# Kernel optimization log

Measured on AMD Instinct MI355X. Metric: run time of the kernel, lower is better.

Reference implementation:

```python
import jax, jax.numpy as jnp
import numpy as np

NF = 64  # n_features
NL = 3   # n_layers


def setup_inputs() -> dict:
    key = jax.random.key(0)
    ks = jax.random.split(key, 16)
    B, G, P = 4, 512, 512
    obs = jax.random.randint(ks[0], (B, G, P), 0, 3).astype(jnp.float32)

    def w(k, shape, fan_in):
        return (jax.random.normal(k, shape, jnp.float32) / np.sqrt(fan_in)).astype(jnp.float32)

    return {
        "obs": obs,
        "W_init_g": w(ks[1], (1, NF), 1),          # node_init_embedding_layer_g Linear(1,64)
        "W_init_p": w(ks[2], (1, NF), 1),
        "W_ee_g": w(ks[3], (1, NF - 1), 1),        # edge_embedding_NN (n_obs_in_p -> 63)
        "W_ef_g": w(ks[4], (NF, NF), NF),          # edge_feature_NN (64 -> 64)
        "W_ee_p": w(ks[5], (1, NF - 1), 1),
        "W_ef_p": w(ks[6], (NF, NF), NF),
        "W_msg_g": w(ks[7], (NL, 2 * NF, NF), 2 * NF),
        "W_upd_g": w(ks[8], (NL, 2 * NF, NF), 2 * NF),
        "W_msg_p": w(ks[9], (NL, 2 * NF, NF), 2 * NF),
        "W_upd_p": w(ks[10], (NL, 2 * NF, NF), 2 * NF),
        "W_pool_g": w(ks[11], (NF, NF), NF),
        "W_pool_p": w(ks[12], (NF, NF), NF),
        "W_ro": w(ks[13], (2 * NF, 1), 2 * NF),    # readout Linear(128,1,bias=True)
        "b_ro": jnp.zeros((1,), jnp.float32),
    }


def _norms(a):
    # torch get_normalisation is under no_grad
    n = jax.lax.stop_gradient(jnp.sum(a != 0, axis=-1, keepdims=True).astype(a.dtype))
    return n, jnp.where(n == 0, 1.0, n)


def _edge_emb(node_feat_opp, adj, norm, nf1, W_ee, W_ef):
    # node_feat_opp: [B,C,1], adj: [B,R,C] -> edge tensor [B,R,C,1]
    mask = (adj != 0).astype(adj.dtype)
    ef = node_feat_opp[:, None, :, :] * mask[..., None]          # [B,R,C,1]
    ee = jax.nn.relu(jnp.einsum('brci,ie->brce', ef, W_ee))      # [B,R,C,63]
    emb = ee.sum(axis=2) / nf1                                   # [B,R,63]
    x = jnp.concatenate([emb, norm / jnp.max(nf1)], axis=-1)     # [B,R,64]
    return jax.nn.relu(x @ W_ef)


def reference(obs, W_init_g, W_init_p, W_ee_g, W_ef_g, W_ee_p, W_ef_p,
              W_msg_g, W_upd_g, W_msg_p, W_upd_p, W_pool_g, W_pool_p, W_ro, b_ro):
    relu = jax.nn.relu
    adj = obs                                  # n_obs_in_g == 1 -> no leading node features
    adjT = jnp.swapaxes(adj, -1, -2)
    B, G, P = adj.shape
    norm_g, nf1_g = _norms(adj)
    norm_p, nf1_p = _norms(adjT)
    nf_g = norm_g / P                          # node_features_g [B,G,1]
    nf_p = norm_p / G                          # node_features_p [B,P,1]
    h_g = relu(nf_g @ W_init_g)                # [B,G,64]
    h_p = relu(nf_p @ W_init_p)                # [B,P,64]
    e_g = _edge_emb(nf_p, adj, norm_g, nf1_g, W_ee_g, W_ef_g)
    e_p = _edge_emb(nf_g, adjT, norm_p, nf1_p, W_ee_p, W_ef_p)
    for i in range(NL):
        agg_g = (adj @ h_p) / nf1_g
        agg_p = (adjT @ h_g) / nf1_p
        m_g = relu(jnp.concatenate([agg_g, e_g], axis=-1) @ W_msg_g[i])
        m_p = relu(jnp.concatenate([agg_p, e_p], axis=-1) @ W_msg_p[i])
        h_g_new = relu(jnp.concatenate([h_g, m_g], axis=-1) @ W_upd_g[i])
        h_p_new = relu(jnp.concatenate([h_p, m_p], axis=-1) @ W_upd_p[i])
        h_g, h_p = h_g_new, h_p_new
    hp_g = (h_g.sum(axis=1) / G) @ W_pool_g    # [B,64]
    hp_p = (h_p.sum(axis=1) / P) @ W_pool_p
    hp = relu(hp_g + hp_p)
    f_pooled = jnp.broadcast_to(hp[:, None, :], h_g.shape)
    feats = relu(jnp.concatenate([f_pooled, h_g], axis=-1))      # [B,G,128]
    out = feats @ W_ro + b_ro                  # [B,G,1]
    return out[..., 0]                         # torch .squeeze() -> [B,G]
```

## Files before the change

kernel.cpp:

```cpp
#include <hip/hip_runtime.h>

#define NF 64

#define OFF_U       8194
#define OFF_NPG     9216
#define OFF_NPP     25600
#define OFF_HA_G    41984
#define OFF_HA_P    173056
#define OFF_HB_G    304128
#define OFF_HB_P    435200
#define OFF_EG      566272
#define OFF_EP      697344
#define OFF_AFRAG   2162688
#define OFF_HFA     3211264
#define OFF_HFB     3735552
#define OFF_WF      4259840
#define OFF_HPART   4358144

typedef __attribute__((ext_vector_type(8))) short bf16x8;
typedef __attribute__((ext_vector_type(4))) float f32x4;

static __device__ __forceinline__ float wave_sum(float v) {
    for (int off = 32; off; off >>= 1) v += __shfl_down(v, off, 64);
    return v;
}
static __device__ __forceinline__ float wave_max(float v) {
    for (int off = 32; off; off >>= 1) v = fmaxf(v, __shfl_down(v, off, 64));
    return v;
}
static __device__ __forceinline__ unsigned short f2bf(float x) {
    unsigned u = __float_as_uint(x);
    return (unsigned short)((u + 0x7FFFu + ((u >> 16) & 1u)) >> 16);
}

__global__ __launch_bounds__(256) void k_prep(const float* __restrict__ obs,
        float* __restrict__ ws,
        const float* __restrict__ Wm_g, const float* __restrict__ Wu_g,
        const float* __restrict__ Wm_p, const float* __restrict__ Wu_p,
        const float* __restrict__ Wee_g, const float* __restrict__ Wef_g,
        const float* __restrict__ Wee_p, const float* __restrict__ Wef_p) {
    __shared__ float tile[64][65];
    __shared__ float cc[4][64];
    int b = blockIdx.y, t = threadIdx.x;
    int tg = blockIdx.x >> 3, tp = blockIdx.x & 7;
    int g0 = tg * 64, p0 = tp * 64;
    int c = t & 63, q = t >> 6;
    const float* src = obs + ((size_t)b * 512 + g0) * 512 + p0;
    float colcnt = 0.f;
#pragma unroll
    for (int i = 0; i < 16; ++i) {
        int r = q + 4 * i;
        float v = src[(size_t)r * 512 + c];
        tile[r][c] = v;
        bool nz = (v != 0.f);
        colcnt += nz ? 1.f : 0.f;
        unsigned long long mask = __ballot(nz);
        if (c == 0)
            ws[OFF_NPG + tp * 2048 + b * 512 + g0 + r] = (float)__popcll(mask);
    }
    cc[q][c] = colcnt;
    __syncthreads();
    if (q == 0)
        ws[OFF_NPP + tg * 2048 + b * 512 + p0 + c] =
            cc[0][c] + cc[1][c] + cc[2][c] + cc[3][c];
    int ri = c & 15, kq = c >> 4;
    unsigned short* afg = (unsigned short*)(ws + OFF_AFRAG);
    unsigned short* afp = afg + 1048576;
    int rt_g = b * 32 + tg * 4 + q;
    int rt_p = b * 32 + tp * 4 + q;
#pragma unroll
    for (int ks2 = 0; ks2 < 2; ++ks2) {
        int ks_g = tp * 2 + ks2;
        int ks_p = tg * 2 + ks2;
        bf16x8 og, op;
#pragma unroll
        for (int i = 0; i < 8; ++i) {
            og[i] = (short)f2bf(tile[q * 16 + ri][ks2 * 32 + kq * 8 + i]);
            op[i] = (short)f2bf(tile[ks2 * 32 + kq * 8 + i][q * 16 + ri]);
        }
        *(bf16x8*)(afg + ((size_t)(rt_g * 16 + ks_g) * 64 + c) * 8) = og;
        *(bf16x8*)(afp + ((size_t)(rt_p * 16 + ks_p) * 64 + c) * 8) = op;
    }
    int lin = b * 64 + blockIdx.x;
    if (lin < 48) {
        int mat = lin >> 2, ks2 = lin & 3;
        int side = mat / 6, m = (mat / 3) & 1, layer = mat % 3;
        const float* W = (side ? (m ? Wu_p : Wm_p) : (m ? Wu_g : Wm_g)) + layer * 8192;
        int ftq = t >> 6, lane = t & 63;
        int f = ftq * 16 + (lane & 15);
        int kbase = ks2 * 32 + ((lane >> 4) & 3) * 8;
        bf16x8 oh, ol;
#pragma unroll
        for (int i = 0; i < 8; ++i) {
            float v = W[(kbase + i) * 64 + f];
            unsigned short hi = f2bf(v);
            oh[i] = (short)hi;
            ol[i] = (short)f2bf(v - __uint_as_float((unsigned)hi << 16));
        }
        unsigned short* WF = (unsigned short*)(ws + OFF_WF);
        *(bf16x8*)(WF + (((size_t)(mat * 2 + 0) * 4 + ks2) * 4 + ftq) * 512 + lane * 8) = oh;
        *(bf16x8*)(WF + (((size_t)(mat * 2 + 1) * 4 + ks2) * 4 + ftq) * 512 + lane * 8) = ol;
    } else if (lin == 48 && t < 128) {
        int side = t >> 6, f = t & 63;
        const float* Wee = side ? Wee_p : Wee_g;
        const float* Wef = side ? Wef_p : Wef_g;
        float u = 0.f;
#pragma unroll
        for (int e = 0; e < 63; ++e) u += fmaxf(Wee[e], 0.f) * Wef[e * 64 + f];
        ws[OFF_U + t] = u;
    }
}

__global__ __launch_bounds__(256) void k_init(float* __restrict__ ws,
        const float* __restrict__ Wi_g, const float* __restrict__ Wi_p,
        const float* __restrict__ Wef_g, const float* __restrict__ Wef_p) {
    __shared__ float normall[2048];
    __shared__ float nopp[512];
    __shared__ float redm[4];
    __shared__ float sred[4][16];
    __shared__ float s_l[16];
    int bid = blockIdx.x, side = bid >> 7, rt = bid & 127;
    int lr0 = rt * 16, b = rt >> 5;
    int t = threadIdx.x, lane = t & 63, w = t >> 6;
    const float* pown = ws + (side ? OFF_NPP : OFF_NPG);
    const float* popp = ws + (side ? OFF_NPG : OFF_NPP) + b * 512;
#pragma unroll
    for (int i = 0; i < 8; ++i) {
        int r = t + 256 * i;
        float s = 0.f;
#pragma unroll
        for (int j = 0; j < 8; ++j) s += pown[j * 2048 + r];
        normall[r] = s;
    }
#pragma unroll
    for (int i = 0; i < 2; ++i) {
        int r = t + 256 * i;
        float s = 0.f;
#pragma unroll
        for (int j = 0; j < 8; ++j) s += popp[j * 2048 + r];
        nopp[r] = s;
    }
    __syncthreads();
    float m = 0.f;
#pragma unroll
    for (int i = 0; i < 8; ++i) m = fmaxf(m, normall[t + 256 * i]);
    m = wave_max(m);
    if (lane == 0) redm[w] = m;
    const unsigned short* af = (const unsigned short*)(ws + OFF_AFRAG)
                               + (size_t)side * 1048576;
    int kq = lane >> 4;
    float sacc = 0.f;
#pragma unroll
    for (int kk = 0; kk < 4; ++kk) {
        int ks = w * 4 + kk;
        bf16x8 a = *(const bf16x8*)(af + ((size_t)(rt * 16 + ks) * 64 + lane) * 8);
#pragma unroll
        for (int i = 0; i < 8; ++i)
            if (a[i] != 0) sacc += nopp[ks * 32 + kq * 8 + i];
    }
    sacc += __shfl_xor(sacc, 16, 64);
    sacc += __shfl_xor(sacc, 32, 64);
    if (lane < 16) sred[w][lane] = sacc;
    __syncthreads();
    float mxs = fmaxf(fmaxf(redm[0], redm[1]), fmaxf(redm[2], redm[3]));
    if (t < 16)
        s_l[t] = (sred[0][t] + sred[1][t] + sred[2][t] + sred[3][t]) * (1.f / 512.f);
    __syncthreads();
    float maxnf = fmaxf(mxs, 1.f);
    const float* Wi = side ? Wi_p : Wi_g;
    const float* Wef = side ? Wef_p : Wef_g;
    int ff = lane;
    float Uv = ws[OFF_U + side * 64 + ff];
    float wef63 = Wef[63 * 64 + ff];
    float wiv = Wi[ff];
    unsigned short hi4[4], lo4[4];
#pragma unroll
    for (int q = 0; q < 4; ++q) {
        int r = w * 4 + q, lr = lr0 + r;
        float norm = normall[lr];
        float nf1 = norm > 0.f ? norm : 1.f;
        float h = fmaxf(norm * (1.f / 512.f) * wiv, 0.f);
        ws[(side ? OFF_HA_P : OFF_HA_G) + (size_t)lr * 64 + ff] = h;
        unsigned short hh = f2bf(h);
        hi4[q] = hh;
        lo4[q] = f2bf(h - __uint_as_float((unsigned)hh << 16));
        float A = s_l[r] / nf1;
        float C = norm / maxnf;
        float e = fmaxf(A * Uv + C * wef63, 0.f);
        ws[(side ? OFF_EP : OFF_EG) + (size_t)lr * 64 + ff] = e;
    }
    int k0 = (rt & 31) * 16 + w * 4;
    int ks_h = k0 >> 5;
    int lane2 = (ff & 15) | (((k0 >> 3) & 3) << 4);
    int ft = ff >> 4;
    size_t fidx = (((size_t)(b * 4 + ft) * 16 + ks_h) * 64 + lane2) * 8 + (k0 & 7);
    unsigned short* hf = (unsigned short*)(ws + OFF_HFA) + (size_t)side * 2 * 262144;
    uint2 vh, vl;
    vh.x = (unsigned)hi4[0] | ((unsigned)hi4[1] << 16);
    vh.y = (unsigned)hi4[2] | ((unsigned)hi4[3] << 16);
    vl.x = (unsigned)lo4[0] | ((unsigned)lo4[1] << 16);
    vl.y = (unsigned)lo4[2] | ((unsigned)lo4[3] << 16);
    *(uint2*)(hf + fidx) = vh;
    *(uint2*)(hf + 262144 + fidx) = vl;
}

__global__ __launch_bounds__(256) void k_layer(float* __restrict__ ws, int layer,
        int hin_g, int hin_p, int hout_g, int hout_p, int fin, int fout, int do_pool) {
    __shared__ float xe[16][68], xh[16][68], xa[16][68], xm[16][68];
    __shared__ float nrm16[16];
    __shared__ float psum[4][64];
    int bid = blockIdx.x, side = bid >> 7, rt = bid & 127;
    int lr0 = rt * 16, b = rt >> 5;
    int t = threadIdx.x, lane = t & 63;
    int ft = __builtin_amdgcn_readfirstlane(t >> 6);

    {
        int r = t >> 4, c4 = (t & 15) * 4;
        *(float4*)&xe[r][c4] = *(const float4*)(ws + (side ? OFF_EP : OFF_EG)
                                                + (size_t)(lr0 + r) * 64 + c4);
        *(float4*)&xh[r][c4] = *(const float4*)(ws + (side ? hin_p : hin_g)
                                                + (size_t)(lr0 + r) * 64 + c4);
        if (t < 16) {
            const float* po = ws + (side ? OFF_NPP : OFF_NPG) + lr0 + t;
            float s = 0.f;
#pragma unroll
            for (int j = 0; j < 8; ++j) s += po[j * 2048];
            nrm16[t] = fmaxf(s, 1.f);
        }
    }
    __syncthreads();

    const unsigned short* af = (const unsigned short*)(ws + OFF_AFRAG)
                               + (size_t)side * 1048576;
    const unsigned short* hfh = (const unsigned short*)(ws + fin)
                                + (size_t)(1 - side) * 2 * 262144;
    const unsigned short* hfl = hfh + 262144;
    f32x4 acc = {0.f, 0.f, 0.f, 0.f};
#pragma unroll
    for (int ks = 0; ks < 16; ++ks) {
        bf16x8 a = *(const bf16x8*)(af + ((size_t)(rt * 16 + ks) * 64 + lane) * 8);
        size_t bi = ((((size_t)b * 4 + ft) * 16 + ks) * 64 + lane) * 8;
        bf16x8 bh = *(const bf16x8*)(hfh + bi);
        bf16x8 bl = *(const bf16x8*)(hfl + bi);
        acc = __builtin_amdgcn_mfma_f32_16x16x32_bf16(a, bh, acc, 0, 0, 0);
        acc = __builtin_amdgcn_mfma_f32_16x16x32_bf16(a, bl, acc, 0, 0, 0);
    }
    {
        int c = lane & 15, rq = (lane >> 4) * 4, f = ft * 16 + c;
#pragma unroll
        for (int j = 0; j < 4; ++j)
            xa[rq + j][f] = acc[j] / nrm16[rq + j];
    }
    __syncthreads();

    const unsigned short* WF = (const unsigned short*)(ws + OFF_WF);
    int mat_msg = (side * 2 + 0) * 3 + layer;
    int mat_upd = (side * 2 + 1) * 3 + layer;
    int ar = lane & 15, koff = ((lane >> 4) & 3) * 8;

    f32x4 mc = {0.f, 0.f, 0.f, 0.f};
#pragma unroll
    for (int ks2 = 0; ks2 < 4; ++ks2) {
        const float* src = (ks2 < 2) ? &xa[ar][ks2 * 32 + koff]
                                     : &xe[ar][(ks2 - 2) * 32 + koff];
        float4 lo4 = *(const float4*)src;
        float4 hi4 = *(const float4*)(src + 4);
        bf16x8 xhf, xlf;
        {
            float xv[8] = {lo4.x, lo4.y, lo4.z, lo4.w, hi4.x, hi4.y, hi4.z, hi4.w};
#pragma unroll
            for (int i = 0; i < 8; ++i) {
                unsigned short hh = f2bf(xv[i]);
                xhf[i] = (short)hh;
                xlf[i] = (short)f2bf(xv[i] - __uint_as_float((unsigned)hh << 16));
            }
        }
        bf16x8 wh = *(const bf16x8*)(WF + (((size_t)(mat_msg * 2 + 0) * 4 + ks2) * 4 + ft) * 512 + lane * 8);
        bf16x8 wl = *(const bf16x8*)(WF + (((size_t)(mat_msg * 2 + 1) * 4 + ks2) * 4 + ft) * 512 + lane * 8);
        mc = __builtin_amdgcn_mfma_f32_16x16x32_bf16(xhf, wh, mc, 0, 0, 0);
        mc = __builtin_amdgcn_mfma_f32_16x16x32_bf16(xlf, wh, mc, 0, 0, 0);
        mc = __builtin_amdgcn_mfma_f32_16x16x32_bf16(xhf, wl, mc, 0, 0, 0);
    }
    {
        int c = lane & 15, rq = (lane >> 4) * 4, f = ft * 16 + c;
#pragma unroll
        for (int j = 0; j < 4; ++j) xm[rq + j][f] = fmaxf(mc[j], 0.f);
    }
    __syncthreads();

    f32x4 uc = {0.f, 0.f, 0.f, 0.f};
#pragma unroll
    for (int ks2 = 0; ks2 < 4; ++ks2) {
        const float* src = (ks2 < 2) ? &xh[ar][ks2 * 32 + koff]
                                     : &xm[ar][(ks2 - 2) * 32 + koff];
        float4 lo4 = *(const float4*)src;
        float4 hi4 = *(const float4*)(src + 4);
        bf16x8 xhf, xlf;
        {
            float xv[8] = {lo4.x, lo4.y, lo4.z, lo4.w, hi4.x, hi4.y, hi4.z, hi4.w};
#pragma unroll
            for (int i = 0; i < 8; ++i) {
                unsigned short hh = f2bf(xv[i]);
                xhf[i] = (short)hh;
                xlf[i] = (short)f2bf(xv[i] - __uint_as_float((unsigned)hh << 16));
            }
        }
        bf16x8 wh = *(const bf16x8*)(WF + (((size_t)(mat_upd * 2 + 0) * 4 + ks2) * 4 + ft) * 512 + lane * 8);
        bf16x8 wl = *(const bf16x8*)(WF + (((size_t)(mat_upd * 2 + 1) * 4 + ks2) * 4 + ft) * 512 + lane * 8);
        uc = __builtin_amdgcn_mfma_f32_16x16x32_bf16(xhf, wh, uc, 0, 0, 0);
        uc = __builtin_amdgcn_mfma_f32_16x16x32_bf16(xlf, wh, uc, 0, 0, 0);
        uc = __builtin_amdgcn_mfma_f32_16x16x32_bf16(xhf, wl, uc, 0, 0, 0);
    }
    {
        int c = lane & 15, rq = (lane >> 4) * 4, f = ft * 16 + c;
        int hout = side ? hout_p : hout_g;
        float s4 = 0.f;
        unsigned short hi4[4], lo4[4];
#pragma unroll
        for (int j = 0; j < 4; ++j) {
            float hv = fmaxf(uc[j], 0.f);
            ws[hout + (size_t)(lr0 + rq + j) * 64 + f] = hv;
            unsigned short hh = f2bf(hv);
            hi4[j] = hh;
            lo4[j] = f2bf(hv - __uint_as_float((unsigned)hh << 16));
            s4 += hv;
        }
        int k0 = (rt & 31) * 16 + rq;
        int ks_h = k0 >> 5;
        int lane2 = (f & 15) | (((k0 >> 3) & 3) << 4);
        size_t fidx = (((size_t)(b * 4 + ft) * 16 + ks_h) * 64 + lane2) * 8 + (k0 & 7);
        unsigned short* hf = (unsigned short*)(ws + fout) + (size_t)side * 2 * 262144;
        uint2 vh, vl;
        vh.x = (unsigned)hi4[0] | ((unsigned)hi4[1] << 16);
        vh.y = (unsigned)hi4[2] | ((unsigned)hi4[3] << 16);
        vl.x = (unsigned)lo4[0] | ((unsigned)lo4[1] << 16);
        vl.y = (unsigned)lo4[2] | ((unsigned)lo4[3] << 16);
        *(uint2*)(hf + fidx) = vh;
        *(uint2*)(hf + 262144 + fidx) = vl;
        if (do_pool) {
            psum[lane >> 4][f] = s4;
            __syncthreads();
            if (t < 64)
                ws[OFF_HPART + bid * 64 + t] =
                    psum[0][t] + psum[1][t] + psum[2][t] + psum[3][t];
        }
    }
}

__global__ __launch_bounds__(256) void k_out(const float* __restrict__ Wpg,
                                             const float* __restrict__ Wpp,
                                             const float* __restrict__ Wro,
                                             const float* __restrict__ bro,
                                             const float* __restrict__ ws,
                                             float* __restrict__ out) {
    __shared__ float hp[128];
    __shared__ float c1s;
    int bid = blockIdx.x;
    int row0 = bid * 256, b = row0 >> 9;
    int t = threadIdx.x;
    if (t < 128) {
        int sd = t >> 6, k = t & 63;
        const float* q = ws + OFF_HPART + (size_t)(sd * 128 + b * 32) * 64 + k;
        float s = 0.f;
#pragma unroll
        for (int i = 0; i < 32; ++i) s += q[i * 64];
        hp[t] = s;
    }
    __syncthreads();
    if (t < 64) {
        float vg = 0.f, vp = 0.f;
#pragma unroll 4
        for (int k = 0; k < 64; ++k) {
            vg += (hp[k] * (1.f / 512.f)) * Wpg[k * 64 + t];
            vp += (hp[64 + k] * (1.f / 512.f)) * Wpp[k * 64 + t];
        }
        float hv = fmaxf(vg + vp, 0.f);
        float c = wave_sum(hv * Wro[t]);
        if (t == 0) c1s = c + bro[0];
    }
    __syncthreads();
    int idx = row0 + t;
    const float4* hrow = (const float4*)(ws + OFF_HB_G + (size_t)idx * 64);
    float s = 0.f;
#pragma unroll
    for (int k4 = 0; k4 < 16; ++k4) {
        float4 h4 = hrow[k4];
        s += h4.x * Wro[64 + k4 * 4 + 0];
        s += h4.y * Wro[64 + k4 * 4 + 1];
        s += h4.z * Wro[64 + k4 * 4 + 2];
        s += h4.w * Wro[64 + k4 * 4 + 3];
    }
    out[idx] = c1s + s;
}

extern "C" void kernel_launch(void* const* d_in, const int* in_sizes, int n_in,
                              void* d_out, int out_size, void* d_ws, size_t ws_size,
                              hipStream_t stream) {
    const float* obs   = (const float*)d_in[0];
    const float* Wi_g  = (const float*)d_in[1];
    const float* Wi_p  = (const float*)d_in[2];
    const float* Wee_g = (const float*)d_in[3];
    const float* Wef_g = (const float*)d_in[4];
    const float* Wee_p = (const float*)d_in[5];
    const float* Wef_p = (const float*)d_in[6];
    const float* Wm_g  = (const float*)d_in[7];
    const float* Wu_g  = (const float*)d_in[8];
    const float* Wm_p  = (const float*)d_in[9];
    const float* Wu_p  = (const float*)d_in[10];
    const float* Wpg   = (const float*)d_in[11];
    const float* Wpp   = (const float*)d_in[12];
    const float* Wro   = (const float*)d_in[13];
    const float* bro   = (const float*)d_in[14];
    float* ws  = (float*)d_ws;
    float* out = (float*)d_out;

    k_prep<<<dim3(64, 4), 256, 0, stream>>>(obs, ws, Wm_g, Wu_g, Wm_p, Wu_p,
                                            Wee_g, Wef_g, Wee_p, Wef_p);
    k_init<<<256, 256, 0, stream>>>(ws, Wi_g, Wi_p, Wef_g, Wef_p);

    k_layer<<<256, 256, 0, stream>>>(ws, 0, OFF_HA_G, OFF_HA_P, OFF_HB_G, OFF_HB_P,
                                     OFF_HFA, OFF_HFB, 0);
    k_layer<<<256, 256, 0, stream>>>(ws, 1, OFF_HB_G, OFF_HB_P, OFF_HA_G, OFF_HA_P,
                                     OFF_HFB, OFF_HFA, 0);
    k_layer<<<256, 256, 0, stream>>>(ws, 2, OFF_HA_G, OFF_HA_P, OFF_HB_G, OFF_HB_P,
                                     OFF_HFA, OFF_HFB, 1);

    k_out<<<8, 256, 0, stream>>>(Wpg, Wpp, Wro, bro, ws, out);
}
```

Baseline: 54.31 us.

## Fuse layer 0 into init using rank-one structure of initial embeddings

Because the initial node embeddings are relu(norm/N * W_init), the layer-0 aggregation adj @ h_opp reduces to a weighted sum of opposite-side norms times relu(W_init_opp). That scalar is accumulated alongside the existing edge-embedding reduction, and the layer-0 message and update MFMA matmuls run inside the init kernel. This removes one full layer kernel and its adjacency matmul and launch. It assumes the opposite initial embedding is rank-one, which holds because the norms are non-negative.

Measured after the change: 46.88 us, median of 2. -13.7%, faster.

```diff
diff --git a/kernel.cpp b/kernel.cpp
--- a/kernel.cpp
+++ b/kernel.cpp
@@ -111,14 +111,15 @@
     }
 }
 
-__global__ __launch_bounds__(256) void k_init(float* __restrict__ ws,
+__global__ __launch_bounds__(256) void k_init_l0(float* __restrict__ ws,
         const float* __restrict__ Wi_g, const float* __restrict__ Wi_p,
         const float* __restrict__ Wef_g, const float* __restrict__ Wef_p) {
     __shared__ float normall[2048];
     __shared__ float nopp[512];
     __shared__ float redm[4];
-    __shared__ float sred[4][16];
-    __shared__ float s_l[16];
+    __shared__ float sred[4][16], wred[4][16];
+    __shared__ float s_l[16], w_l[16];
+    __shared__ float xe[16][68], xh[16][68], xa[16][68], xm[16][68];
     int bid = blockIdx.x, side = bid >> 7, rt = bid & 127;
     int lr0 = rt * 16, b = rt >> 5;
     int t = threadIdx.x, lane = t & 63, w = t >> 6;
@@ -149,59 +150,141 @@
     const unsigned short* af = (const unsigned short*)(ws + OFF_AFRAG)
                                + (size_t)side * 1048576;
     int kq = lane >> 4;
-    float sacc = 0.f;
+    float sacc = 0.f, wacc = 0.f;
 #pragma unroll
     for (int kk = 0; kk < 4; ++kk) {
         int ks = w * 4 + kk;
         bf16x8 a = *(const bf16x8*)(af + ((size_t)(rt * 16 + ks) * 64 + lane) * 8);
 #pragma unroll
         for (int i = 0; i < 8; ++i)
-            if (a[i] != 0) sacc += nopp[ks * 32 + kq * 8 + i];
+            if (a[i] != 0) {
+                float nv = nopp[ks * 32 + kq * 8 + i];
+                sacc += nv;
+                float av = __uint_as_float((unsigned)(unsigned short)a[i] << 16);
+                wacc += av * nv;
+            }
     }
     sacc += __shfl_xor(sacc, 16, 64);
     sacc += __shfl_xor(sacc, 32, 64);
-    if (lane < 16) sred[w][lane] = sacc;
+    wacc += __shfl_xor(wacc, 16, 64);
+    wacc += __shfl_xor(wacc, 32, 64);
+    if (lane < 16) { sred[w][lane] = sacc; wred[w][lane] = wacc; }
     __syncthreads();
     float mxs = fmaxf(fmaxf(redm[0], redm[1]), fmaxf(redm[2], redm[3]));
-    if (t < 16)
+    if (t < 16) {
         s_l[t] = (sred[0][t] + sred[1][t] + sred[2][t] + sred[3][t]) * (1.f / 512.f);
+        w_l[t] = (wred[0][t] + wred[1][t] + wred[2][t] + wred[3][t]) * (1.f / 512.f);
+    }
     __syncthreads();
     float maxnf = fmaxf(mxs, 1.f);
-    const float* Wi = side ? Wi_p : Wi_g;
+    const float* Wi_own = side ? Wi_p : Wi_g;
+    const float* Wi_opp = side ? Wi_g : Wi_p;
     const float* Wef = side ? Wef_p : Wef_g;
     int ff = lane;
     float Uv = ws[OFF_U + side * 64 + ff];
     float wef63 = Wef[63 * 64 + ff];
-    float wiv = Wi[ff];
-    unsigned short hi4[4], lo4[4];
+    float wiv = Wi_own[ff];
+    float wio = fmaxf(Wi_opp[ff], 0.f);
 #pragma unroll
     for (int q = 0; q < 4; ++q) {
         int r = w * 4 + q, lr = lr0 + r;
         float norm = normall[lr];
         float nf1 = norm > 0.f ? norm : 1.f;
         float h = fmaxf(norm * (1.f / 512.f) * wiv, 0.f);
-        ws[(side ? OFF_HA_P : OFF_HA_G) + (size_t)lr * 64 + ff] = h;
-        unsigned short hh = f2bf(h);
-        hi4[q] = hh;
-        lo4[q] = f2bf(h - __uint_as_float((unsigned)hh << 16));
+        xh[r][ff] = h;
         float A = s_l[r] / nf1;
         float C = norm / maxnf;
         float e = fmaxf(A * Uv + C * wef63, 0.f);
         ws[(side ? OFF_EP : OFF_EG) + (size_t)lr * 64 + ff] = e;
-    }
-    int k0 = (rt & 31) * 16 + w * 4;
-    int ks_h = k0 >> 5;
-    int lane2 = (ff & 15) | (((k0 >> 3) & 3) << 4);
-    int ft = ff >> 4;
-    size_t fidx = (((size_t)(b * 4 + ft) * 16 + ks_h) * 64 + lane2) * 8 + (k0 & 7);
-    unsigned short* hf = (unsigned short*)(ws + OFF_HFA) + (size_t)side * 2 * 262144;
-    uint2 vh, vl;
-    vh.x = (unsigned)hi4[0] | ((unsigned)hi4[1] << 16);
-    vh.y = (unsigned)hi4[2] | ((unsigned)hi4[3] << 16);
-    vl.x = (unsigned)lo4[0] | ((unsigned)lo4[1] << 16);
-    vl.y = (unsigned)lo4[2] | ((unsigned)lo4[3] << 16);
-    *(uint2*)(hf + fidx) = vh;
-    *(uint2*)(hf + 262144 + fidx) = vl;
+        xe[r][ff] = e;
+        xa[r][ff] = w_l[r] * wio / nf1;
+    }
+    __syncthreads();
+
+    int ft = __builtin_amdgcn_readfirstlane(w);
+    const unsigned short* WF = (const unsigned short*)(ws + OFF_WF);
+    int mat_msg = (side * 2 + 0) * 3 + 0;
+    int mat_upd = (side * 2 + 1) * 3 + 0;
+    int ar = lane & 15, koff = ((lane >> 4) & 3) * 8;
+
+    f32x4 mc = {0.f, 0.f, 0.f, 0.f};
+#pragma unroll
+    for (int ks2 = 0; ks2 < 4; ++ks2) {
+        const float* src = (ks2 < 2) ? &xa[ar][ks2 * 32 + koff]
+                                     : &xe[ar][(ks2 - 2) * 32 + koff];
+        float4 lo4 = *(const float4*)src;
+        float4 hi4 = *(const float4*)(src + 4);
+        bf16x8 xhf, xlf;
+        {
+            float xv[8] = {lo4.x, lo4.y, lo4.z, lo4.w, hi4.x, hi4.y, hi4.z, hi4.w};
+#pragma unroll
+            for (int i = 0; i < 8; ++i) {
+                unsigned short hh = f2bf(xv[i]);
+                xhf[i] = (short)hh;
+                xlf[i] = (short)f2bf(xv[i] - __uint_as_float((unsigned)hh << 16));
+            }
+        }
+        bf16x8 wh = *(const bf16x8*)(WF + (((size_t)(mat_msg * 2 + 0) * 4 + ks2) * 4 + ft) * 512 + lane * 8);
+        bf16x8 wl = *(const bf16x8*)(WF + (((size_t)(mat_msg * 2 + 1) * 4 + ks2) * 4 + ft) * 512 + lane * 8);
+        mc = __builtin_amdgcn_mfma_f32_16x16x32_bf16(xhf, wh, mc, 0, 0, 0);
+        mc = __builtin_amdgcn_mfma_f32_16x16x32_bf16(xlf, wh, mc, 0, 0, 0);
+        mc = __builtin_amdgcn_mfma_f32_16x16x32_bf16(xhf, wl, mc, 0, 0, 0);
+    }
+    {
+        int c = lane & 15, rq = (lane >> 4) * 4, f = ft * 16 + c;
+#pragma unroll
+        for (int j = 0; j < 4; ++j) xm[rq + j][f] = fmaxf(mc[j], 0.f);
+    }
+    __syncthreads();
+
+    f32x4 uc = {0.f, 0.f, 0.f, 0.f};
+#pragma unroll
+    for (int ks2 = 0; ks2 < 4; ++ks2) {
+        const float* src = (ks2 < 2) ? &xh[ar][ks2 * 32 + koff]
+                                     : &xm[ar][(ks2 - 2) * 32 + koff];
+        float4 lo4 = *(const float4*)src;
+        float4 hi4 = *(const float4*)(src + 4);
+        bf16x8 xhf, xlf;
+        {
+            float xv[8] = {lo4.x, lo4.y, lo4.z, lo4.w, hi4.x, hi4.y, hi4.z, hi4.w};
+#pragma unroll
+            for (int i = 0; i < 8; ++i) {
+                unsigned short hh = f2bf(xv[i]);
+                xhf[i] = (short)hh;
+                xlf[i] = (short)f2bf(xv[i] - __uint_as_float((unsigned)hh << 16));
+            }
+        }
+        bf16x8 wh = *(const bf16x8*)(WF + (((size_t)(mat_upd * 2 + 0) * 4 + ks2) * 4 + ft) * 512 + lane * 8);
+        bf16x8 wl = *(const bf16x8*)(WF + (((size_t)(mat_upd * 2 + 1) * 4 + ks2) * 4 + ft) * 512 + lane * 8);
+        uc = __builtin_amdgcn_mfma_f32_16x16x32_bf16(xhf, wh, uc, 0, 0, 0);
+        uc = __builtin_amdgcn_mfma_f32_16x16x32_bf16(xlf, wh, uc, 0, 0, 0);
+        uc = __builtin_amdgcn_mfma_f32_16x16x32_bf16(xhf, wl, uc, 0, 0, 0);
+    }
+    {
+        int c = lane & 15, rq = (lane >> 4) * 4, f = ft * 16 + c;
+        int hout = side ? OFF_HB_P : OFF_HB_G;
+        unsigned short hi4[4], lo4b[4];
+#pragma unroll
+        for (int j = 0; j < 4; ++j) {
+            float hv = fmaxf(uc[j], 0.f);
+            ws[hout + (size_t)(lr0 + rq + j) * 64 + f] = hv;
+            unsigned short hh = f2bf(hv);
+            hi4[j] = hh;
+            lo4b[j] = f2bf(hv - __uint_as_float((unsigned)hh << 16));
+        }
+        int k0 = (rt & 31) * 16 + rq;
+        int ks_h = k0 >> 5;
+        int lane2 = (f & 15) | (((k0 >> 3) & 3) << 4);
+        size_t fidx = (((size_t)(b * 4 + ft) * 16 + ks_h) * 64 + lane2) * 8 + (k0 & 7);
+        unsigned short* hf = (unsigned short*)(ws + OFF_HFB) + (size_t)side * 2 * 262144;
+        uint2 vh, vl;
+        vh.x = (unsigned)hi4[0] | ((unsigned)hi4[1] << 16);
+        vh.y = (unsigned)hi4[2] | ((unsigned)hi4[3] << 16);
+        vl.x = (unsigned)lo4b[0] | ((unsigned)lo4b[1] << 16);
+        vl.y = (unsigned)lo4b[2] | ((unsigned)lo4b[3] << 16);
+        *(uint2*)(hf + fidx) = vh;
+        *(uint2*)(hf + 262144 + fidx) = vl;
+    }
 }
 
 __global__ __launch_bounds__(256) void k_layer(float* __restrict__ ws, int layer,
@@ -416,10 +499,8 @@
 
     k_prep<<<dim3(64, 4), 256, 0, stream>>>(obs, ws, Wm_g, Wu_g, Wm_p, Wu_p,
                                             Wee_g, Wef_g, Wee_p, Wef_p);
-    k_init<<<256, 256, 0, stream>>>(ws, Wi_g, Wi_p, Wef_g, Wef_p);
-
-    k_layer<<<256, 256, 0, stream>>>(ws, 0, OFF_HA_G, OFF_HA_P, OFF_HB_G, OFF_HB_P,
-                                     OFF_HFA, OFF_HFB, 0);
+    k_init_l0<<<256, 256, 0, stream>>>(ws, Wi_g, Wi_p, Wef_g, Wef_p);
+
     k_layer<<<256, 256, 0, stream>>>(ws, 1, OFF_HB_G, OFF_HB_P, OFF_HA_G, OFF_HA_P,
                                      OFF_HFB, OFF_HFA, 0);
     k_layer<<<256, 256, 0, stream>>>(ws, 2, OFF_HA_G, OFF_HA_P, OFF_HB_G, OFF_HB_P,
```
